# Kernel optimization log

Measured on AMD Instinct MI355X. Metric: run time of the kernel, lower is better.

The kernel has to match this reference:

```python
import jax, jax.numpy as jnp
import numpy as np

B, L, C = 8, 8192, 256
FOCAL_LEVEL = 3
KERNELS = [3, 5, 7]  # focal_factor*k + focal_x[0]
LN_EPS = 1e-3  # keras LayerNormalization default epsilon


def _gelu(x):
    return jax.nn.gelu(x, approximate=False)  # keras 'gelu' is exact


def _layernorm(x, g, b):
    m = jnp.mean(x, axis=-1, keepdims=True)
    v = jnp.var(x, axis=-1, keepdims=True)
    return (x - m) * jax.lax.rsqrt(v + LN_EPS) * g + b


def _conv1d_same(x, w, b):
    # x: [B,L,Cin], w: [K,Cin,Cout]
    y = jax.lax.conv_general_dilated(x, w, window_strides=(1,), padding='SAME',
                                     dimension_numbers=('NWC', 'WIO', 'NWC'))
    return y + b


def setup_inputs() -> dict:
    key = jax.random.key(0)
    ks = jax.random.split(key, 16)
    s = 0.02
    inp = {
        'x': jax.random.normal(ks[0], (B, L, C), dtype=jnp.float32),
        'f_w': jax.random.normal(ks[1], (C, 2 * C + FOCAL_LEVEL + 1), dtype=jnp.float32) * s,
        'f_b': jnp.zeros((2 * C + FOCAL_LEVEL + 1,), dtype=jnp.float32),
        'h_w': jax.random.normal(ks[2], (1, C, C), dtype=jnp.float32) * s,
        'h_b': jnp.zeros((C,), dtype=jnp.float32),
        'proj_w': jax.random.normal(ks[3], (C, C), dtype=jnp.float32) * s,
        'proj_b': jnp.zeros((C,), dtype=jnp.float32),
    }
    for l, K in enumerate(KERNELS):
        inp[f'conv_w{l}'] = jax.random.normal(ks[4 + l], (K, C, C), dtype=jnp.float32) * s
        inp[f'conv_b{l}'] = jnp.zeros((C,), dtype=jnp.float32)
        inp[f'ln_g{l}'] = jnp.ones((C,), dtype=jnp.float32)
        inp[f'ln_b{l}'] = jnp.zeros((C,), dtype=jnp.float32)
    return inp


def reference(x, f_w, f_b,
              conv_w0, conv_b0, ln_g0, ln_b0,
              conv_w1, conv_b1, ln_g1, ln_b1,
              conv_w2, conv_b2, ln_g2, ln_b2,
              h_w, h_b, proj_w, proj_b):
    x_fea = x @ f_w + f_b                      # [B,L,2C+4]
    q = x_fea[..., :C]
    ctx = x_fea[..., C:2 * C]
    gates = x_fea[..., 2 * C:]                 # [B,L,4]

    levels = [(conv_w0, conv_b0, ln_g0, ln_b0),
              (conv_w1, conv_b1, ln_g1, ln_b1),
              (conv_w2, conv_b2, ln_g2, ln_b2)]

    ctx_all = jnp.zeros_like(ctx)
    for l, (cw, cb, lg, lb) in enumerate(levels):
        ctx = _layernorm(_gelu(_conv1d_same(ctx, cw, cb)), lg, lb)
        ctx_all = ctx_all + ctx * gates[..., l:l + 1]

    # global average pool gate (broadcasts over L)
    ctx_global = jnp.mean(ctx, axis=1, keepdims=True) * gates[..., FOCAL_LEVEL:]
    ctx_all = ctx_all + ctx_global

    # h: 1x1 conv == dense
    ctx_all = jnp.einsum('blc,cd->bld', ctx_all, h_w[0]) + h_b
    x_out = (q * ctx_all) @ proj_w + proj_b    # proj_drop is identity at inference
    return x_out
```

## Files before the change

### kernel.cpp

```cpp
#include <hip/hip_runtime.h>
#include <math.h>

#define CDIM 256
#define LSEQ 8192
#define BATCH 8
#define MTOT (BATCH * LSEQ)
#define PADROWS 8208
#define PAD0 8

typedef unsigned short ushort_t;
typedef unsigned int uint_t;

typedef __bf16 bf16x8 __attribute__((ext_vector_type(8)));
typedef float f32x4 __attribute__((ext_vector_type(4)));

__device__ __forceinline__ ushort_t f2bf(float f) {
    union { float f; uint_t u; } v; v.f = f;
    uint_t u = v.u;
    return (ushort_t)((u + 0x7FFFu + ((u >> 16) & 1u)) >> 16);
}
__device__ __forceinline__ float bf2f(ushort_t h) {
    union { uint_t u; float f; } v; v.u = ((uint_t)h) << 16;
    return v.f;
}
__device__ __forceinline__ float gelu_exact(float x) {
    return 0.5f * x * (1.0f + erff(x * 0.70710678118654752440f));
}

__device__ __forceinline__ void gload16(const ushort_t* g, ushort_t* lds) {
    __builtin_amdgcn_global_load_lds(
        reinterpret_cast<__attribute__((address_space(1))) uint_t*>(
            reinterpret_cast<uintptr_t>(g)),
        reinterpret_cast<__attribute__((address_space(3))) uint_t*>(
            reinterpret_cast<uintptr_t>(lds)),
        16, 0, 0);
}

__global__ __launch_bounds__(256) void cvt_gates(
    const float* __restrict__ x, const float* __restrict__ f_w,
    const float* __restrict__ f_b,
    ushort_t* __restrict__ x_bf, float* __restrict__ gates)
{
    __shared__ float fcol[256][4];
    int tid = threadIdx.x;
    #pragma unroll
    for (int j = 0; j < 4; ++j) fcol[tid][j] = f_w[(size_t)tid * 516 + 512 + j];
    __syncthreads();
    int w = tid >> 6, l = tid & 63;
    size_t t = (size_t)blockIdx.x * 4 + w;
    float4 xv = ((const float4*)(x + t * CDIM))[l];
    ((ushort4*)(x_bf + t * CDIM))[l] =
        make_ushort4(f2bf(xv.x), f2bf(xv.y), f2bf(xv.z), f2bf(xv.w));
    int c = l * 4;
    float a[4];
    #pragma unroll
    for (int j = 0; j < 4; ++j)
        a[j] = xv.x * fcol[c][j] + xv.y * fcol[c + 1][j] + xv.z * fcol[c + 2][j] + xv.w * fcol[c + 3][j];
    #pragma unroll
    for (int off = 32; off >= 1; off >>= 1)
        #pragma unroll
        for (int j = 0; j < 4; ++j) a[j] += __shfl_xor(a[j], off);
    if (l == 0) {
        #pragma unroll
        for (int j = 0; j < 4; ++j) gates[t * 4 + j] = a[j] + f_b[512 + j];
    }
}

__global__ __launch_bounds__(256) void prep_weights(
    const float* __restrict__ f_w,  const float* __restrict__ c0,
    const float* __restrict__ c1,   const float* __restrict__ c2,
    const float* __restrict__ h_w,  const float* __restrict__ p_w,
    ushort_t* __restrict__ f_wT, ushort_t* __restrict__ c0T,
    ushort_t* __restrict__ c1T,  ushort_t* __restrict__ c2T,
    ushort_t* __restrict__ h_wT, ushort_t* __restrict__ p_wT)
{
    __shared__ float t[32][33];
    int r = blockIdx.x;
    const float* in; ushort_t* out; int Kt, ldin;
    if (r < 128)              { in = f_w; out = f_wT; Kt = 8;  ldin = 516; }
    else if ((r -= 128) < 192){ in = c0;  out = c0T;  Kt = 24; ldin = 256; }
    else if ((r -= 192) < 320){ in = c1;  out = c1T;  Kt = 40; ldin = 256; }
    else if ((r -= 320) < 448){ in = c2;  out = c2T;  Kt = 56; ldin = 256; }
    else if ((r -= 448) < 64) { in = h_w; out = h_wT; Kt = 8;  ldin = 256; }
    else                      { r -= 64; in = p_w; out = p_wT; Kt = 8; ldin = 256; }
    int K = Kt * 32;
    int k0 = (r % Kt) * 32, n0 = (r / Kt) * 32;
    int tx = threadIdx.x & 31, ty = threadIdx.x >> 5;
    #pragma unroll
    for (int i = 0; i < 4; i++) {
        int k = k0 + ty + i * 8;
        t[ty + i * 8][tx] = in[(size_t)k * ldin + n0 + tx];
    }
    __syncthreads();
    #pragma unroll
    for (int i = 0; i < 4; i++) {
        int n = n0 + ty + i * 8;
        out[(size_t)n * K + k0 + tx] = f2bf(t[tx][ty + i * 8]);
    }
}

__global__ __launch_bounds__(256) void zero_guards_all(ushort_t* __restrict__ ctx_base) {
    int i = blockIdx.x * 256 + threadIdx.x;
    int buf = i >> 15;
    int j = i & 32767;
    int c = j & 255;
    int rr = (j >> 8) & 15;
    int b = j >> 12;
    size_t row = (size_t)b * PADROWS + ((rr < 8) ? rr : (PADROWS - 16 + rr));
    ctx_base[((size_t)buf * BATCH * PADROWS + row) * CDIM + c] = 0;
}

template <int MODE>
__global__ __launch_bounds__(256) void gemm_bf16(
    const ushort_t* __restrict__ A, const ushort_t* __restrict__ BT,
    const float* __restrict__ bias,
    float* __restrict__ C, ushort_t* __restrict__ q_out, ushort_t* __restrict__ ctx_pad,
    int Ktot)
{
    __shared__ __align__(16) ushort_t As[128 * 32];
    __shared__ __align__(16) ushort_t Bs[128 * 32];
    int tid = threadIdx.x;
    int w = tid >> 6, l = tid & 63;
    int bn = blockIdx.x * 128;
    int by = blockIdx.y;
    long arow0 = (long)by * 128;
    int crow0 = by * 128;

    int wr = w >> 1, wc = w & 1;
    int lr = l & 15, lk = (l >> 4) * 8;
    int sr = l >> 2;
    int sc = (l & 3) * 8;

    f32x4 acc[4][4] = {};

    int nsteps = Ktot >> 5;
    for (int kt = 0; kt < nsteps; ++kt) {
        int k0 = kt << 5;
        #pragma unroll
        for (int jj = 0; jj < 2; ++jj) {
            int j = w * 2 + jj;
            int r = j * 16 + sr;
            gload16(A + (arow0 + r) * CDIM + (k0 + sc), &As[j * 512]);
            gload16(BT + (long)(bn + r) * Ktot + (k0 + sc), &Bs[j * 512]);
        }
        __syncthreads();
        bf16x8 av[4], bv[4];
        #pragma unroll
        for (int m = 0; m < 4; ++m)
            av[m] = *reinterpret_cast<const bf16x8*>(&As[(wr * 64 + m * 16 + lr) * 32 + lk]);
        #pragma unroll
        for (int n = 0; n < 4; ++n)
            bv[n] = *reinterpret_cast<const bf16x8*>(&Bs[(wc * 64 + n * 16 + lr) * 32 + lk]);
        #pragma unroll
        for (int m = 0; m < 4; ++m)
            #pragma unroll
            for (int n = 0; n < 4; ++n)
                acc[m][n] = __builtin_amdgcn_mfma_f32_16x16x32_bf16(av[m], bv[n], acc[m][n], 0, 0, 0);
        __syncthreads();
    }

    int rbase = (l >> 4) * 4;
    #pragma unroll
    for (int n = 0; n < 4; ++n) {
        int col = bn + wc * 64 + n * 16 + lr;
        float bia = bias[col];
        #pragma unroll
        for (int m = 0; m < 4; ++m) {
            int rowb = crow0 + wr * 64 + m * 16 + rbase;
            #pragma unroll
            for (int r = 0; r < 4; ++r) {
                float v = acc[m][n][r] + bia;
                int row = rowb + r;
                if (MODE == 0) {
                    C[(size_t)row * CDIM + col] = v;
                } else if (MODE == 1) {
                    if (col < CDIM) {
                        q_out[(size_t)row * CDIM + col] = f2bf(v);
                    } else {
                        int bb = row >> 13, tb = row & (LSEQ - 1);
                        ctx_pad[((size_t)bb * PADROWS + PAD0 + tb) * CDIM + (col - CDIM)] = f2bf(v);
                    }
                } else {
                    size_t idx = (size_t)row * CDIM + col;
                    q_out[idx] = f2bf(bf2f(q_out[idx]) * v);
                }
            }
        }
    }
}

__device__ __forceinline__ void stageA128(const ushort_t* Arow0, int cc,
                                          ushort_t* asb, int tid, int w) {
    int row = tid >> 2, cp = tid & 3;
    int cg = cp ^ ((row >> 1) & 3);
    gload16(Arow0 + (size_t)row * CDIM + cc * 32 + cg * 8, asb + (size_t)(w * 64) * 8);
    if (tid < 64) {
        int o2 = 512 + tid;
        int row2 = o2 >> 2, cp2 = o2 & 3;
        int cg2 = cp2 ^ ((row2 >> 1) & 3);
        gload16(Arow0 + (size_t)row2 * CDIM + cc * 32 + cg2 * 8, asb + (size_t)512 * 8);
    }
}
__device__ __forceinline__ void stageB128(const ushort_t* BT, int Ktot, int koffB,
                                          ushort_t* bsb, int tid) {
    #pragma unroll
    for (int i = 0; i < 2; ++i) {
        int o = tid + i * 512;
        int n = o >> 2, cp = o & 3;
        int cg = cp ^ ((n >> 1) & 3);
        gload16(BT + (size_t)n * Ktot + koffB + cg * 8,
                bsb + (size_t)((o >> 6) * 64) * 8);
    }
}

__global__ __launch_bounds__(512, 4) void conv_fused(
    const ushort_t* __restrict__ A, const ushort_t* __restrict__ BT,
    const float* __restrict__ bias,
    const float* __restrict__ lng, const float* __restrict__ lnb,
    ushort_t* __restrict__ ctx_out, int KW, int Ktot)
{
    __shared__ __align__(16) ushort_t As2[2][144 * 32];
    __shared__ __align__(16) ushort_t Bs[2][256 * 32];

    int tid = threadIdx.x;
    int w = tid >> 6, l = tid & 63;
    int by = blockIdx.x;
    int b = by >> 6;
    int tloc = (by & 63) << 7;
    const ushort_t* Arow0 = A + ((size_t)b * PADROWS + PAD0 + tloc - 8) * CDIM;

    int wr = w >> 2;
    int wc = w & 3;
    int lr = l & 15;
    int quad = l >> 4;

    int P = KW >> 1;
    int hoff = 8 - P;
    f32x4 acc[4][4] = {};

    stageA128(Arow0, 0, As2[0], tid, w);
    stageB128(BT, Ktot, 0, Bs[0], tid);
    __syncthreads();

    int nIt = KW * 8;
    int it = 0;
    for (int c = 0; c < 8; ++c) {
        for (int tap = 0; tap < KW; ++tap, ++it) {
            if (tap == 0 && c < 7)
                stageA128(Arow0, c + 1, As2[(c + 1) & 1], tid, w);
            if (it + 1 < nIt) {
                int tapn = tap + 1, cn = c;
                if (tapn == KW) { tapn = 0; cn = c + 1; }
                stageB128(BT, Ktot, tapn * 256 + cn * 32, Bs[(it + 1) & 1], tid);
            }
            const ushort_t* asb = As2[c & 1];
            const ushort_t* bsb = Bs[it & 1];
            bf16x8 av[4], bv[4];
            #pragma unroll
            for (int m = 0; m < 4; ++m) {
                int row = wr * 64 + m * 16 + lr + tap + hoff;
                int cs = quad ^ ((row >> 1) & 3);
                av[m] = *reinterpret_cast<const bf16x8*>(&asb[row * 32 + cs * 8]);
            }
            #pragma unroll
            for (int n = 0; n < 4; ++n) {
                int nn = wc * 64 + n * 16 + lr;
                int cs = quad ^ ((nn >> 1) & 3);
                bv[n] = *reinterpret_cast<const bf16x8*>(&bsb[nn * 32 + cs * 8]);
            }
            #pragma unroll
            for (int m = 0; m < 4; ++m)
                #pragma unroll
                for (int n = 0; n < 4; ++n)
                    acc[m][n] = __builtin_amdgcn_mfma_f32_16x16x32_bf16(av[m], bv[n], acc[m][n], 0, 0, 0);
            __syncthreads();
        }
    }

    float* rs = (float*)&Bs[0][0];
    float* rq = rs + 512;
    float bias_c[4], lng_c[4], lnb_c[4];
    #pragma unroll
    for (int n = 0; n < 4; ++n) {
        int col = wc * 64 + n * 16 + lr;
        bias_c[n] = bias[col];
        lng_c[n] = lng[col];
        lnb_c[n] = lnb[col];
    }
    #pragma unroll
    for (int m = 0; m < 4; ++m) {
        #pragma unroll
        for (int r = 0; r < 4; ++r) {
            float s = 0.0f, sq = 0.0f;
            #pragma unroll
            for (int n = 0; n < 4; ++n) {
                float v = acc[m][n][r] + bias_c[n];
                v = gelu_exact(v);
                acc[m][n][r] = v;
                s += v; sq += v * v;
            }
            s += __shfl_xor(s, 1);  sq += __shfl_xor(sq, 1);
            s += __shfl_xor(s, 2);  sq += __shfl_xor(sq, 2);
            s += __shfl_xor(s, 4);  sq += __shfl_xor(sq, 4);
            s += __shfl_xor(s, 8);  sq += __shfl_xor(sq, 8);
            if (lr == 0) {
                int rl = wr * 64 + m * 16 + quad * 4 + r;
                rs[rl * 4 + wc] = s;
                rq[rl * 4 + wc] = sq;
            }
        }
    }
    __syncthreads();
    #pragma unroll
    for (int m = 0; m < 4; ++m) {
        #pragma unroll
        for (int r = 0; r < 4; ++r) {
            int rl = wr * 64 + m * 16 + quad * 4 + r;
            float mean = (rs[rl * 4] + rs[rl * 4 + 1] + rs[rl * 4 + 2] + rs[rl * 4 + 3]) * (1.0f / 256.0f);
            float var = (rq[rl * 4] + rq[rl * 4 + 1] + rq[rl * 4 + 2] + rq[rl * 4 + 3]) * (1.0f / 256.0f) - mean * mean;
            float inv = rsqrtf(var + 1e-3f);
            int trow = tloc + rl;
            ushort_t* cp = ctx_out + ((size_t)b * PADROWS + PAD0 + trow) * CDIM;
            #pragma unroll
            for (int n = 0; n < 4; ++n) {
                int col = wc * 64 + n * 16 + lr;
                float y = (acc[m][n][r] - mean) * inv * lng_c[n] + lnb_c[n];
                cp[col] = f2bf(y);
            }
        }
    }
}

__global__ __launch_bounds__(256) void col_mean_partial(const ushort_t* __restrict__ ctx_pad,
                                                        float* __restrict__ partial) {
    int b = blockIdx.x, chunk = blockIdx.y, c = threadIdx.x;
    const ushort_t* base = ctx_pad + ((size_t)b * PADROWS + PAD0 + chunk * 256) * CDIM + c;
    float s = 0.0f;
    for (int r = 0; r < 256; ++r) s += bf2f(base[(size_t)r * CDIM]);
    partial[((size_t)b * 32 + chunk) * CDIM + c] = s;
}

__global__ __launch_bounds__(256) void col_mean_final(const float* __restrict__ partial,
                                                      float* __restrict__ meanv) {
    int b = blockIdx.x, c = threadIdx.x;
    float s = 0.0f;
    for (int i = 0; i < 32; ++i) s += partial[((size_t)b * 32 + i) * CDIM + c];
    meanv[b * CDIM + c] = s * (1.0f / (float)LSEQ);
}

__global__ __launch_bounds__(256) void finalize_A(
    const ushort_t* __restrict__ c0buf, const ushort_t* __restrict__ c1buf,
    const ushort_t* __restrict__ c2buf,
    const float* __restrict__ meanv, const float* __restrict__ gates,
    ushort_t* __restrict__ A_bf)
{
    int i = blockIdx.x * 256 + threadIdx.x;
    int t = i >> 5;
    int c8 = (i & 31) * 8;
    int b = t >> 13, tb = t & (LSEQ - 1);
    size_t pidx = ((size_t)b * PADROWS + PAD0 + tb) * CDIM + c8;
    const float* g = gates + (size_t)t * 4;
    float g0 = g[0], g1 = g[1], g2 = g[2], g3 = g[3];
    ushort4 a0 = *(const ushort4*)(c0buf + pidx);
    ushort4 a1 = *(const ushort4*)(c0buf + pidx + 4);
    ushort4 b0 = *(const ushort4*)(c1buf + pidx);
    ushort4 b1 = *(const ushort4*)(c1buf + pidx + 4);
    ushort4 d0 = *(const ushort4*)(c2buf + pidx);
    ushort4 d1 = *(const ushort4*)(c2buf + pidx + 4);
    const float* mv = meanv + b * CDIM + c8;
    ushort_t out[8];
    ushort_t va[8] = { a0.x, a0.y, a0.z, a0.w, a1.x, a1.y, a1.z, a1.w };
    ushort_t vb[8] = { b0.x, b0.y, b0.z, b0.w, b1.x, b1.y, b1.z, b1.w };
    ushort_t vd[8] = { d0.x, d0.y, d0.z, d0.w, d1.x, d1.y, d1.z, d1.w };
    #pragma unroll
    for (int j = 0; j < 8; ++j) {
        float v = bf2f(va[j]) * g0 + bf2f(vb[j]) * g1 + bf2f(vd[j]) * g2 + mv[j] * g3;
        out[j] = f2bf(v);
    }
    *(ushort4*)(A_bf + (size_t)t * CDIM + c8)     = make_ushort4(out[0], out[1], out[2], out[3]);
    *(ushort4*)(A_bf + (size_t)t * CDIM + c8 + 4) = make_ushort4(out[4], out[5], out[6], out[7]);
}

extern "C" void kernel_launch(void* const* d_in, const int* in_sizes, int n_in,
                              void* d_out, int out_size, void* d_ws, size_t ws_size,
                              hipStream_t stream) {
    const float* x      = (const float*)d_in[0];
    const float* f_w    = (const float*)d_in[1];
    const float* f_b    = (const float*)d_in[2];
    const float* h_w    = (const float*)d_in[3];
    const float* h_b    = (const float*)d_in[4];
    const float* proj_w = (const float*)d_in[5];
    const float* proj_b = (const float*)d_in[6];
    const float* conv_w[3] = { (const float*)d_in[7],  (const float*)d_in[11], (const float*)d_in[15] };
    const float* conv_b[3] = { (const float*)d_in[8],  (const float*)d_in[12], (const float*)d_in[16] };
    const float* ln_g[3]   = { (const float*)d_in[9],  (const float*)d_in[13], (const float*)d_in[17] };
    const float* ln_b[3]   = { (const float*)d_in[10], (const float*)d_in[14], (const float*)d_in[18] };

    const size_t MC = (size_t)MTOT * CDIM;
    const size_t PADC = (size_t)BATCH * PADROWS * CDIM;
    char* w = (char*)d_ws;
    ushort_t* x_bf  = (ushort_t*)w;  w += MC * 2;
    ushort_t* q_bf  = (ushort_t*)w;  w += MC * 2;
    ushort_t* ctxF  = (ushort_t*)w;  w += PADC * 2;
    ushort_t* ctx0  = (ushort_t*)w;  w += PADC * 2;
    ushort_t* ctx1  = (ushort_t*)w;  w += PADC * 2;
    ushort_t* ctx2  = (ushort_t*)w;  w += PADC * 2;
    float* gates    = (float*)w;     w += (size_t)MTOT * 4 * 4;
    float* partial  = (float*)w;     w += (size_t)8 * 32 * CDIM * 4;
    float* meanv    = (float*)w;     w += (size_t)8 * CDIM * 4;
    ushort_t* f_wT  = (ushort_t*)w;  w += (size_t)512 * 256 * 2;
    ushort_t* convT0 = (ushort_t*)w; w += (size_t)768 * 256 * 2;
    ushort_t* convT1 = (ushort_t*)w; w += (size_t)1280 * 256 * 2;
    ushort_t* convT2 = (ushort_t*)w; w += (size_t)1792 * 256 * 2;
    ushort_t* h_wT   = (ushort_t*)w; w += (size_t)256 * 256 * 2;
    ushort_t* proj_wT = (ushort_t*)w; w += (size_t)256 * 256 * 2;
    ushort_t* A_bf = x_bf;

    dim3 blk(256);

    cvt_gates<<<dim3(MTOT / 4), blk, 0, stream>>>(x, f_w, f_b, x_bf, gates);
    prep_weights<<<dim3(1216), blk, 0, stream>>>(f_w, conv_w[0], conv_w[1], conv_w[2],
        h_w, proj_w, f_wT, convT0, convT1, convT2, h_wT, proj_wT);
    zero_guards_all<<<dim3(512), blk, 0, stream>>>(ctxF);

    gemm_bf16<1><<<dim3(4, 512), blk, 0, stream>>>(x_bf, f_wT, f_b,
        nullptr, q_bf, ctxF, 256);

    conv_fused<<<dim3(512), dim3(512), 0, stream>>>(ctxF, convT0, conv_b[0],
        ln_g[0], ln_b[0], ctx0, 3, 768);
    conv_fused<<<dim3(512), dim3(512), 0, stream>>>(ctx0, convT1, conv_b[1],
        ln_g[1], ln_b[1], ctx1, 5, 1280);
    conv_fused<<<dim3(512), dim3(512), 0, stream>>>(ctx1, convT2, conv_b[2],
        ln_g[2], ln_b[2], ctx2, 7, 1792);

    col_mean_partial<<<dim3(BATCH, 32), blk, 0, stream>>>(ctx2, partial);
    col_mean_final<<<dim3(BATCH), blk, 0, stream>>>(partial, meanv);

    finalize_A<<<dim3(MTOT * 32 / 256), blk, 0, stream>>>(ctx0, ctx1, ctx2,
        meanv, gates, A_bf);

    gemm_bf16<2><<<dim3(2, 512), blk, 0, stream>>>(A_bf, h_wT, h_b,
        nullptr, q_bf, nullptr, 256);
    gemm_bf16<0><<<dim3(2, 512), blk, 0, stream>>>(q_bf, proj_wT, proj_b,
        (float*)d_out, nullptr, nullptr, 256);
}
```

Measured before the change: 373.9 us.

## Fuse gated context combine, h GEMM, q multiply and proj GEMM into one kernel

Replaces the finalize_A kernel and two separate GEMM launches with a single tail kernel. Each 512-thread block computes the gated sum of the three context levels and the global mean directly into shared memory as the A tile, runs the h GEMM, multiplies by q, and stores the bf16 product in a swizzled 64KB shared buffer. It then runs the proj GEMM from that buffer and writes the output. This removes the A_bf and q*ctx round trips through global memory and two launches, at the cost of large shared memory use (80KB), which lowers occupancy, and serialized per-block GEMM phases.

```diff
diff --git a/kernel.cpp b/kernel.cpp
--- a/kernel.cpp
+++ b/kernel.cpp
@@ -110,12 +110,10 @@
     ctx_base[((size_t)buf * BATCH * PADROWS + row) * CDIM + c] = 0;
 }
 
-template <int MODE>
-__global__ __launch_bounds__(256) void gemm_bf16(
+__global__ __launch_bounds__(256) void fea_gemm(
     const ushort_t* __restrict__ A, const ushort_t* __restrict__ BT,
     const float* __restrict__ bias,
-    float* __restrict__ C, ushort_t* __restrict__ q_out, ushort_t* __restrict__ ctx_pad,
-    int Ktot)
+    ushort_t* __restrict__ q_out, ushort_t* __restrict__ ctx_pad)
 {
     __shared__ __align__(16) ushort_t As[128 * 32];
     __shared__ __align__(16) ushort_t Bs[128 * 32];
@@ -133,15 +131,14 @@
 
     f32x4 acc[4][4] = {};
 
-    int nsteps = Ktot >> 5;
-    for (int kt = 0; kt < nsteps; ++kt) {
+    for (int kt = 0; kt < 8; ++kt) {
         int k0 = kt << 5;
         #pragma unroll
         for (int jj = 0; jj < 2; ++jj) {
             int j = w * 2 + jj;
             int r = j * 16 + sr;
             gload16(A + (arow0 + r) * CDIM + (k0 + sc), &As[j * 512]);
-            gload16(BT + (long)(bn + r) * Ktot + (k0 + sc), &Bs[j * 512]);
+            gload16(BT + (long)(bn + r) * 256 + (k0 + sc), &Bs[j * 512]);
         }
         __syncthreads();
         bf16x8 av[4], bv[4];
@@ -171,18 +168,11 @@
             for (int r = 0; r < 4; ++r) {
                 float v = acc[m][n][r] + bia;
                 int row = rowb + r;
-                if (MODE == 0) {
-                    C[(size_t)row * CDIM + col] = v;
-                } else if (MODE == 1) {
-                    if (col < CDIM) {
-                        q_out[(size_t)row * CDIM + col] = f2bf(v);
-                    } else {
-                        int bb = row >> 13, tb = row & (LSEQ - 1);
-                        ctx_pad[((size_t)bb * PADROWS + PAD0 + tb) * CDIM + (col - CDIM)] = f2bf(v);
-                    }
+                if (col < CDIM) {
+                    q_out[(size_t)row * CDIM + col] = f2bf(v);
                 } else {
-                    size_t idx = (size_t)row * CDIM + col;
-                    q_out[idx] = f2bf(bf2f(q_out[idx]) * v);
+                    int bb = row >> 13, tb = row & (LSEQ - 1);
+                    ctx_pad[((size_t)bb * PADROWS + PAD0 + tb) * CDIM + (col - CDIM)] = f2bf(v);
                 }
             }
         }
@@ -348,37 +338,149 @@
     meanv[b * CDIM + c] = s * (1.0f / (float)LSEQ);
 }
 
-__global__ __launch_bounds__(256) void finalize_A(
-    const ushort_t* __restrict__ c0buf, const ushort_t* __restrict__ c1buf,
-    const ushort_t* __restrict__ c2buf,
-    const float* __restrict__ meanv, const float* __restrict__ gates,
-    ushort_t* __restrict__ A_bf)
+__global__ __launch_bounds__(512) void tail_fused(
+    const ushort_t* __restrict__ ctx0, const ushort_t* __restrict__ ctx1,
+    const ushort_t* __restrict__ ctx2,
+    const float* __restrict__ gates, const float* __restrict__ meanv,
+    const ushort_t* __restrict__ q_bf,
+    const ushort_t* __restrict__ h_wT, const float* __restrict__ h_b,
+    const ushort_t* __restrict__ proj_wT, const float* __restrict__ proj_b,
+    float* __restrict__ out)
 {
-    int i = blockIdx.x * 256 + threadIdx.x;
-    int t = i >> 5;
-    int c8 = (i & 31) * 8;
-    int b = t >> 13, tb = t & (LSEQ - 1);
-    size_t pidx = ((size_t)b * PADROWS + PAD0 + tb) * CDIM + c8;
-    const float* g = gates + (size_t)t * 4;
-    float g0 = g[0], g1 = g[1], g2 = g[2], g3 = g[3];
-    ushort4 a0 = *(const ushort4*)(c0buf + pidx);
-    ushort4 a1 = *(const ushort4*)(c0buf + pidx + 4);
-    ushort4 b0 = *(const ushort4*)(c1buf + pidx);
-    ushort4 b1 = *(const ushort4*)(c1buf + pidx + 4);
-    ushort4 d0 = *(const ushort4*)(c2buf + pidx);
-    ushort4 d1 = *(const ushort4*)(c2buf + pidx + 4);
-    const float* mv = meanv + b * CDIM + c8;
-    ushort_t out[8];
-    ushort_t va[8] = { a0.x, a0.y, a0.z, a0.w, a1.x, a1.y, a1.z, a1.w };
-    ushort_t vb[8] = { b0.x, b0.y, b0.z, b0.w, b1.x, b1.y, b1.z, b1.w };
-    ushort_t vd[8] = { d0.x, d0.y, d0.z, d0.w, d1.x, d1.y, d1.z, d1.w };
-    #pragma unroll
-    for (int j = 0; j < 8; ++j) {
-        float v = bf2f(va[j]) * g0 + bf2f(vb[j]) * g1 + bf2f(vd[j]) * g2 + mv[j] * g3;
-        out[j] = f2bf(v);
-    }
-    *(ushort4*)(A_bf + (size_t)t * CDIM + c8)     = make_ushort4(out[0], out[1], out[2], out[3]);
-    *(ushort4*)(A_bf + (size_t)t * CDIM + c8 + 4) = make_ushort4(out[4], out[5], out[6], out[7]);
+    __shared__ __align__(16) char pool[81920];
+    ushort_t* As1 = (ushort_t*)pool;
+    ushort_t* Bs1 = (ushort_t*)(pool + 8192);
+    ushort_t* QC  = (ushort_t*)pool;
+    ushort_t* Bs2 = (ushort_t*)(pool + 65536);
+
+    int tid = threadIdx.x;
+    int w = tid >> 6, l = tid & 63;
+    long grow0 = (long)blockIdx.x * 128;
+
+    int wr = w >> 2;
+    int wc = w & 3;
+    int lr = l & 15;
+    int quad = l >> 4;
+    int lk = quad * 8;
+
+    int arow = tid >> 2;
+    int seg = tid & 3;
+    long grow_st = grow0 + arow;
+    int b_st = (int)(grow_st >> 13), tb_st = (int)(grow_st & (LSEQ - 1));
+    size_t prow = ((size_t)b_st * PADROWS + PAD0 + tb_st) * CDIM;
+    float4 gv = *(const float4*)(gates + grow_st * 4);
+
+    f32x4 acc[4][4] = {};
+
+    for (int kt = 0; kt < 8; ++kt) {
+        int col = kt * 32 + seg * 8;
+        ushort4 a0 = *(const ushort4*)(ctx0 + prow + col);
+        ushort4 a1 = *(const ushort4*)(ctx0 + prow + col + 4);
+        ushort4 b0 = *(const ushort4*)(ctx1 + prow + col);
+        ushort4 b1 = *(const ushort4*)(ctx1 + prow + col + 4);
+        ushort4 d0 = *(const ushort4*)(ctx2 + prow + col);
+        ushort4 d1 = *(const ushort4*)(ctx2 + prow + col + 4);
+        float4 m0 = *(const float4*)(meanv + b_st * CDIM + col);
+        float4 m1 = *(const float4*)(meanv + b_st * CDIM + col + 4);
+        ushort_t va[8] = { a0.x, a0.y, a0.z, a0.w, a1.x, a1.y, a1.z, a1.w };
+        ushort_t vb[8] = { b0.x, b0.y, b0.z, b0.w, b1.x, b1.y, b1.z, b1.w };
+        ushort_t vd[8] = { d0.x, d0.y, d0.z, d0.w, d1.x, d1.y, d1.z, d1.w };
+        float mv[8] = { m0.x, m0.y, m0.z, m0.w, m1.x, m1.y, m1.z, m1.w };
+        ushort_t ov[8];
+        #pragma unroll
+        for (int j = 0; j < 8; ++j)
+            ov[j] = f2bf(bf2f(va[j]) * gv.x + bf2f(vb[j]) * gv.y +
+                         bf2f(vd[j]) * gv.z + mv[j] * gv.w);
+        *(ushort4*)(As1 + arow * 32 + seg * 8)     = make_ushort4(ov[0], ov[1], ov[2], ov[3]);
+        *(ushort4*)(As1 + arow * 32 + seg * 8 + 4) = make_ushort4(ov[4], ov[5], ov[6], ov[7]);
+        #pragma unroll
+        for (int i = 0; i < 2; ++i) {
+            int o = tid + i * 512;
+            int n = o >> 2, cp = o & 3;
+            gload16(h_wT + (size_t)n * 256 + kt * 32 + cp * 8,
+                    Bs1 + (size_t)((o >> 6) * 64) * 8);
+        }
+        __syncthreads();
+        bf16x8 av[4], bv[4];
+        #pragma unroll
+        for (int m = 0; m < 4; ++m)
+            av[m] = *reinterpret_cast<const bf16x8*>(&As1[(wr * 64 + m * 16 + lr) * 32 + lk]);
+        #pragma unroll
+        for (int n = 0; n < 4; ++n)
+            bv[n] = *reinterpret_cast<const bf16x8*>(&Bs1[(wc * 64 + n * 16 + lr) * 32 + lk]);
+        #pragma unroll
+        for (int m = 0; m < 4; ++m)
+            #pragma unroll
+            for (int n = 0; n < 4; ++n)
+                acc[m][n] = __builtin_amdgcn_mfma_f32_16x16x32_bf16(av[m], bv[n], acc[m][n], 0, 0, 0);
+        __syncthreads();
+    }
+
+    {
+        float hb_c[4];
+        #pragma unroll
+        for (int n = 0; n < 4; ++n) hb_c[n] = h_b[wc * 64 + n * 16 + lr];
+        #pragma unroll
+        for (int m = 0; m < 4; ++m) {
+            #pragma unroll
+            for (int r = 0; r < 4; ++r) {
+                int row = wr * 64 + m * 16 + quad * 4 + r;
+                long grow = grow0 + row;
+                #pragma unroll
+                for (int n = 0; n < 4; ++n) {
+                    int col = wc * 64 + n * 16 + lr;
+                    float v = acc[m][n][r] + hb_c[n];
+                    float qv = bf2f(q_bf[(size_t)grow * CDIM + col]);
+                    int c16 = (col >> 3) ^ (row & 7);
+                    QC[row * 256 + c16 * 8 + (col & 7)] = f2bf(qv * v);
+                }
+            }
+        }
+    }
+    __syncthreads();
+
+    f32x4 acc2[4][4] = {};
+    for (int kt = 0; kt < 8; ++kt) {
+        #pragma unroll
+        for (int i = 0; i < 2; ++i) {
+            int o = tid + i * 512;
+            int n = o >> 2, cp = o & 3;
+            gload16(proj_wT + (size_t)n * 256 + kt * 32 + cp * 8,
+                    Bs2 + (size_t)((o >> 6) * 64) * 8);
+        }
+        __syncthreads();
+        bf16x8 av[4], bv[4];
+        #pragma unroll
+        for (int m = 0; m < 4; ++m) {
+            int row = wr * 64 + m * 16 + lr;
+            int c16 = (kt * 4 + quad) ^ (row & 7);
+            av[m] = *reinterpret_cast<const bf16x8*>(&QC[row * 256 + c16 * 8]);
+        }
+        #pragma unroll
+        for (int n = 0; n < 4; ++n)
+            bv[n] = *reinterpret_cast<const bf16x8*>(&Bs2[(wc * 64 + n * 16 + lr) * 32 + lk]);
+        #pragma unroll
+        for (int m = 0; m < 4; ++m)
+            #pragma unroll
+            for (int n = 0; n < 4; ++n)
+                acc2[m][n] = __builtin_amdgcn_mfma_f32_16x16x32_bf16(av[m], bv[n], acc2[m][n], 0, 0, 0);
+        __syncthreads();
+    }
+
+    int rbase = quad * 4;
+    #pragma unroll
+    for (int n = 0; n < 4; ++n) {
+        int col = wc * 64 + n * 16 + lr;
+        float pb = proj_b[col];
+        #pragma unroll
+        for (int m = 0; m < 4; ++m) {
+            #pragma unroll
+            for (int r = 0; r < 4; ++r) {
+                long grow = grow0 + wr * 64 + m * 16 + rbase + r;
+                out[(size_t)grow * CDIM + col] = acc2[m][n][r] + pb;
+            }
+        }
+    }
 }
 
 extern "C" void kernel_launch(void* const* d_in, const int* in_sizes, int n_in,
@@ -414,7 +516,6 @@
     ushort_t* convT2 = (ushort_t*)w; w += (size_t)1792 * 256 * 2;
     ushort_t* h_wT   = (ushort_t*)w; w += (size_t)256 * 256 * 2;
     ushort_t* proj_wT = (ushort_t*)w; w += (size_t)256 * 256 * 2;
-    ushort_t* A_bf = x_bf;
 
     dim3 blk(256);
 
@@ -423,8 +524,7 @@
         h_w, proj_w, f_wT, convT0, convT1, convT2, h_wT, proj_wT);
     zero_guards_all<<<dim3(512), blk, 0, stream>>>(ctxF);
 
-    gemm_bf16<1><<<dim3(4, 512), blk, 0, stream>>>(x_bf, f_wT, f_b,
-        nullptr, q_bf, ctxF, 256);
+    fea_gemm<<<dim3(4, 512), blk, 0, stream>>>(x_bf, f_wT, f_b, q_bf, ctxF);
 
     conv_fused<<<dim3(512), dim3(512), 0, stream>>>(ctxF, convT0, conv_b[0],
         ln_g[0], ln_b[0], ctx0, 3, 768);
@@ -436,11 +536,6 @@
     col_mean_partial<<<dim3(BATCH, 32), blk, 0, stream>>>(ctx2, partial);
     col_mean_final<<<dim3(BATCH), blk, 0, stream>>>(partial, meanv);
 
-    finalize_A<<<dim3(MTOT * 32 / 256), blk, 0, stream>>>(ctx0, ctx1, ctx2,
-        meanv, gates, A_bf);
-
-    gemm_bf16<2><<<dim3(2, 512), blk, 0, stream>>>(A_bf, h_wT, h_b,
-        nullptr, q_bf, nullptr, 256);
-    gemm_bf16<0><<<dim3(2, 512), blk, 0, stream>>>(q_bf, proj_wT, proj_b,
-        (float*)d_out, nullptr, nullptr, 256);
-}
+    tail_fused<<<dim3(512), dim3(512), 0, stream>>>(ctx0, ctx1, ctx2,
+        gates, meanv, q_bf, h_wT, h_b, proj_wT, proj_b, (float*)d_out);
+}
```

Result: slower. 388.8 us (+4.0%).
